# Performance work log

Measured on AMD Instinct MI355X. Metric: run time of the kernel, lower is better.

The kernel has to match this reference:

```python
import jax, jax.numpy as jnp
import numpy as np

BETA = 0.25
K = 1024   # num_codebook_vectors
D = 256    # latent_dim


def setup_inputs() -> dict:
    key = jax.random.key(0)
    k1, k2 = jax.random.split(key)
    z = jax.random.normal(k1, (32, D, 32, 32), dtype=jnp.float32)
    # original init: uniform(-1/K, 1/K)
    codebook = jax.random.uniform(k2, (K, D), dtype=jnp.float32, minval=-1.0 / K, maxval=1.0 / K)
    return {"z": z, "codebook": codebook}


def reference(z, codebook):
    B, C, H, W = z.shape
    sg = jax.lax.stop_gradient
    # NCHW -> NHWC, flatten to [N, D]
    z_nhwc = jnp.transpose(z, (0, 2, 3, 1))
    zf = z_nhwc.reshape(-1, C)
    # squared distances via sum-of-squares + matmul: [N, K]
    d = (jnp.sum(zf * zf, axis=1, keepdims=True)
         + jnp.sum(codebook * codebook, axis=1)
         - 2.0 * jnp.matmul(zf, codebook.T))
    idx = jnp.argmin(d, axis=1)                      # [N]
    z_q = codebook[idx].reshape(B, H, W, C)          # gather + reshape
    # commitment + codebook loss
    loss = (jnp.mean((sg(z_q) - z_nhwc) ** 2)
            + BETA * jnp.mean((z_q - sg(z_nhwc)) ** 2))
    # straight-through estimator
    z_q = z_nhwc + sg(z_q - z_nhwc)
    z_q = jnp.transpose(z_q, (0, 3, 1, 2))           # back to NCHW
    return z_q, idx, loss
```

## Files before the change

kernel.cpp:

```cpp
#include <hip/hip_runtime.h>

constexpr int D_ = 256;
constexpr int K_ = 1024;
constexpr int P_ = 1024;
constexpr int N_ = 32768;

constexpr int IDX_OFF  = 8388608;
constexpr int LOSS_OFF = 8421376;

constexpr int CB16_OFF = 0;
constexpr int CN_OFF   = 262400;
constexpr int ZN_OFF   = 263424;
constexpr int CNT_OFF  = 296448;
constexpr int WL_OFF   = 296449;

constexpr float RESCUE_MARGIN = 1e-4f;

typedef _Float16 half8 __attribute__((ext_vector_type(8)));
typedef float f32x4 __attribute__((ext_vector_type(4)));

__device__ __forceinline__ void stage16(const float* g, float* l) {
  __builtin_amdgcn_global_load_lds(
      (const __attribute__((address_space(1))) unsigned int*)g,
      (__attribute__((address_space(3))) unsigned int*)l, 16, 0, 0);
}

__global__ __launch_bounds__(64) void vq_prep(const float* __restrict__ z,
                                              const float* __restrict__ cb,
                                              float* __restrict__ scratch,
                                              float* __restrict__ loss) {
  const int blk = blockIdx.x;
  const int lane = threadIdx.x;
  if (blk < 512) {
    const int n0 = blk * 64;
    const int b = n0 >> 10, p0 = n0 & (P_ - 1);
    const float* zp = z + (size_t)b * (D_ * P_) + p0 + lane;
    float a8[8];
    #pragma unroll
    for (int i = 0; i < 8; ++i) a8[i] = 0.0f;
    for (int oct = 0; oct < 32; ++oct) {
      #pragma unroll
      for (int i = 0; i < 8; ++i) {
        float v = zp[(size_t)(oct * 8 + i) * P_];
        a8[i] = fmaf(v, v, a8[i]);
      }
    }
    scratch[ZN_OFF + n0 + lane] = ((a8[0] + a8[1]) + (a8[2] + a8[3])) +
                                  ((a8[4] + a8[5]) + (a8[6] + a8[7]));
    if (blk == 0 && lane == 0) {
      *loss = 0.0f;
      ((int*)(scratch + CNT_OFF))[0] = 0;
    }
  } else if (blk < 1536) {
    const int k = blk - 512;
    const float* row = cb + (size_t)k * D_;
    double s = 0.0;
    #pragma unroll
    for (int i = 0; i < 4; ++i) {
      double v = (double)row[lane + i * 64];
      s = fma(v, v, s);
    }
    #pragma unroll
    for (int off = 32; off; off >>= 1) s += __shfl_down(s, off, 64);
    if (lane == 0) scratch[CN_OFF + k] = (float)s;
  } else {
    const int kt = blk - 1536;
    const int k = kt * 16 + (lane & 15);
    const int quad = lane >> 4;
    _Float16* cw = (_Float16*)(scratch + CB16_OFF);
    for (int ds = 0; ds < 8; ++ds) {
      const float* src = cb + (size_t)k * D_ + ds * 32 + quad * 8;
      half8 h, lo;
      #pragma unroll
      for (int j = 0; j < 8; ++j) {
        const float v = src[j] * 1024.0f;
        const _Float16 hh = (_Float16)v;
        h[j] = hh;
        lo[j] = (_Float16)(v - (float)hh);
      }
      const int s = kt * 8 + ds;
      *(half8*)(cw + ((size_t)(s * 2 + 0) * 64 + lane) * 8) = h;
      *(half8*)(cw + ((size_t)(s * 2 + 1) * 64 + lane) * 8) = lo;
    }
  }
}

__global__ __launch_bounds__(256, 2) void vq_mfma(const float* __restrict__ z,
                                                  float* __restrict__ scratch,
                                                  float* __restrict__ idxf) {
  const int t = threadIdx.x;
  const int w = t >> 6;
  const int l = t & 63;
  const int quad = l >> 4;
  const int col = l & 15;
  const int n0 = blockIdx.x * 64;
  const int b = n0 >> 10;
  const int p0 = n0 & (P_ - 1);

  const float* __restrict__ cbsw_f = scratch + CB16_OFF;
  const float* __restrict__ cnorm = scratch + CN_OFF;
  const float* __restrict__ zn = scratch + ZN_OFF;

  __shared__ alignas(16) float Bbuf[3][4096];
  __shared__ alignas(16) float cnLds[1024];
  float* Azs = &Bbuf[2][0];

  *(float4*)(cnLds + t * 4) = *(const float4*)(cnorm + t * 4);

  const float4 znv = *(const float4*)(zn + n0 + w * 16 + quad * 4);
  float znr[4] = {znv.x, znv.y, znv.z, znv.w};

  half8 Ah[8], Al[8];
  const int pp = l;
  const int dl0 = w * 8;
  for (int ds = 0; ds < 8; ++ds) {
    __syncthreads();
    #pragma unroll
    for (int i = 0; i < 8; ++i) {
      const int dloc = dl0 + i;
      Azs[pp * 33 + dloc] =
          z[(size_t)b * (D_ * P_) + (size_t)(ds * 32 + dloc) * P_ + p0 + pp];
    }
    __syncthreads();
    {
      const int row_local = w * 16 + col;
      const float* src = &Azs[row_local * 33 + quad * 8];
      half8 h, lo;
      #pragma unroll
      for (int j = 0; j < 8; ++j) {
        const float v = src[j];
        const _Float16 hh = (_Float16)v;
        h[j] = hh;
        lo[j] = (_Float16)(v - (float)hh);
      }
      Ah[ds] = h;
      Al[ds] = lo;
    }
  }

  {
    const float* g0 = cbsw_f + l * 4;
    #pragma unroll
    for (int j = 0; j < 4; ++j) {
      const int chunk = w * 4 + j;
      stage16(g0 + chunk * 256, &Bbuf[0][chunk * 256]);
    }
    #pragma unroll
    for (int j = 0; j < 4; ++j) {
      const int chunk = w * 4 + j;
      stage16(g0 + 4096 + chunk * 256, &Bbuf[1][chunk * 256]);
    }
  }

  float m1[4], m2v[4];
  int i1[4];
  #pragma unroll
  for (int r = 0; r < 4; ++r) { m1[r] = 1e30f; m2v[r] = 1e30f; i1[r] = 0; }

  int cur = 0, stg = 2;
  const float* gs = cbsw_f + 2 * 4096 + l * 4;

  for (int kt = 0; kt < 64; ++kt) {
    if (kt < 63) {
      asm volatile("s_waitcnt vmcnt(4)" ::: "memory");
    } else {
      asm volatile("s_waitcnt vmcnt(0)" ::: "memory");
    }
    __builtin_amdgcn_s_barrier();
    __builtin_amdgcn_sched_barrier(0);

    if (kt < 62) {
      float* db = &Bbuf[stg][0];
      #pragma unroll
      for (int j = 0; j < 4; ++j) {
        const int chunk = w * 4 + j;
        stage16(gs + chunk * 256, db + chunk * 256);
      }
      gs += 4096;
    }

    const float* bb = &Bbuf[cur][0];
    const float cnf = cnLds[(kt << 4) + col];
    f32x4 a0 = {0.f, 0.f, 0.f, 0.f};
    f32x4 a1 = {0.f, 0.f, 0.f, 0.f};

    __builtin_amdgcn_s_setprio(1);
    #pragma unroll
    for (int ds = 0; ds < 4; ++ds) {
      const half8 bh = *(const half8*)(bb + (ds * 2 + 0) * 256 + l * 4);
      const half8 bl = *(const half8*)(bb + (ds * 2 + 1) * 256 + l * 4);
      a0 = __builtin_amdgcn_mfma_f32_16x16x32_f16(Ah[ds], bh, a0, 0, 0, 0);
      a0 = __builtin_amdgcn_mfma_f32_16x16x32_f16(Ah[ds], bl, a0, 0, 0, 0);
      a0 = __builtin_amdgcn_mfma_f32_16x16x32_f16(Al[ds], bh, a0, 0, 0, 0);
    }
    #pragma unroll
    for (int ds = 4; ds < 8; ++ds) {
      const half8 bh = *(const half8*)(bb + (ds * 2 + 0) * 256 + l * 4);
      const half8 bl = *(const half8*)(bb + (ds * 2 + 1) * 256 + l * 4);
      a1 = __builtin_amdgcn_mfma_f32_16x16x32_f16(Ah[ds], bh, a1, 0, 0, 0);
      a1 = __builtin_amdgcn_mfma_f32_16x16x32_f16(Ah[ds], bl, a1, 0, 0, 0);
      a1 = __builtin_amdgcn_mfma_f32_16x16x32_f16(Al[ds], bh, a1, 0, 0, 0);
    }
    __builtin_amdgcn_s_setprio(0);

    const int kg = (kt << 4) + col;
    #pragma unroll
    for (int r = 0; r < 4; ++r) {
      const float s0 = fmaf(a0[r] + a1[r], -0x1p-9f, znr[r] + cnf);
      if (s0 < m1[r]) { m2v[r] = m1[r]; m1[r] = s0; i1[r] = kg; }
      else if (s0 < m2v[r]) m2v[r] = s0;
    }

    cur = (cur == 2) ? 0 : cur + 1;
    stg = (stg == 2) ? 0 : stg + 1;
  }

  #pragma unroll
  for (int off = 1; off <= 8; off <<= 1) {
    #pragma unroll
    for (int r = 0; r < 4; ++r) {
      const float o1 = __shfl_xor(m1[r], off, 64);
      const float o2 = __shfl_xor(m2v[r], off, 64);
      const int oi = __shfl_xor(i1[r], off, 64);
      if (o1 < m1[r]) { m2v[r] = fminf(m1[r], o2); m1[r] = o1; i1[r] = oi; }
      else if (o1 == m1[r]) { i1[r] = min(i1[r], oi); m2v[r] = m1[r]; }
      else { m2v[r] = fminf(m2v[r], o1); }
    }
  }

  if (col == 0) {
    int* cnt = (int*)(scratch + CNT_OFF);
    int* wl = (int*)(scratch + WL_OFF);
    #pragma unroll
    for (int r = 0; r < 4; ++r) {
      const int n = n0 + w * 16 + quad * 4 + r;
      idxf[n] = (float)i1[r];
      if (m2v[r] - m1[r] < RESCUE_MARGIN) {
        const int pos = atomicAdd(cnt, 1);
        wl[pos] = n;
      }
    }
  }
}

__global__ __launch_bounds__(256, 4) void vq_rescue(const float* __restrict__ z,
                                                    const float* __restrict__ cb,
                                                    const float* __restrict__ scratch,
                                                    float* __restrict__ idxf) {
  const int tid = threadIdx.x;
  const float* cnorm = scratch + CN_OFF;
  const float* zn = scratch + ZN_OFF;
  const int count = ((const int*)(scratch + CNT_OFF))[0];
  const int* wl = (const int*)(scratch + WL_OFF);

  __shared__ alignas(16) float zb[8][D_];
  __shared__ int nrow[8];
  __shared__ float rv[256];
  __shared__ int ri[256];

  for (int base = blockIdx.x * 8; base < count; base += gridDim.x * 8) {
    const int take = min(8, count - base);
    if (tid < 8) nrow[tid] = wl[base + (tid < take ? tid : 0)];
    __syncthreads();
    #pragma unroll
    for (int r = 0; r < 8; ++r) {
      const int n = nrow[r];
      const int b = n >> 10, p = n & (P_ - 1);
      zb[r][tid] = z[(size_t)b * (D_ * P_) + (size_t)tid * P_ + p];
    }
    __syncthreads();

    const int k0 = tid * 4;
    const float4* __restrict__ cr0 = (const float4*)(cb + (size_t)(k0 + 0) * D_);
    const float4* __restrict__ cr1 = (const float4*)(cb + (size_t)(k0 + 1) * D_);
    const float4* __restrict__ cr2 = (const float4*)(cb + (size_t)(k0 + 2) * D_);
    const float4* __restrict__ cr3 = (const float4*)(cb + (size_t)(k0 + 3) * D_);

    float acc[8][4];
    #pragma unroll
    for (int r = 0; r < 8; ++r)
      #pragma unroll
      for (int j = 0; j < 4; ++j) acc[r][j] = 0.0f;

    for (int d4 = 0; d4 < 64; ++d4) {
      const float4 v0 = cr0[d4], v1 = cr1[d4], v2 = cr2[d4], v3 = cr3[d4];
      #pragma unroll
      for (int r = 0; r < 8; ++r) {
        const float4 zv = ((const float4*)zb[r])[d4];
        acc[r][0] = fmaf(zv.x, v0.x, acc[r][0]);
        acc[r][0] = fmaf(zv.y, v0.y, acc[r][0]);
        acc[r][0] = fmaf(zv.z, v0.z, acc[r][0]);
        acc[r][0] = fmaf(zv.w, v0.w, acc[r][0]);
        acc[r][1] = fmaf(zv.x, v1.x, acc[r][1]);
        acc[r][1] = fmaf(zv.y, v1.y, acc[r][1]);
        acc[r][1] = fmaf(zv.z, v1.z, acc[r][1]);
        acc[r][1] = fmaf(zv.w, v1.w, acc[r][1]);
        acc[r][2] = fmaf(zv.x, v2.x, acc[r][2]);
        acc[r][2] = fmaf(zv.y, v2.y, acc[r][2]);
        acc[r][2] = fmaf(zv.z, v2.z, acc[r][2]);
        acc[r][2] = fmaf(zv.w, v2.w, acc[r][2]);
        acc[r][3] = fmaf(zv.x, v3.x, acc[r][3]);
        acc[r][3] = fmaf(zv.y, v3.y, acc[r][3]);
        acc[r][3] = fmaf(zv.z, v3.z, acc[r][3]);
        acc[r][3] = fmaf(zv.w, v3.w, acc[r][3]);
      }
    }

    for (int r = 0; r < 8; ++r) {
      const int n = nrow[r];
      const float zA = zn[n];
      float bv = 1e30f;
      int bi = 0x7fffffff;
      #pragma unroll
      for (int j = 0; j < 4; ++j) {
        const float A = zA + cnorm[k0 + j];
        const float s = A - 2.0f * acc[r][j];
        if (s < bv) { bv = s; bi = k0 + j; }
      }
      rv[tid] = bv; ri[tid] = bi;
      __syncthreads();
      for (int off = 128; off >= 1; off >>= 1) {
        if (tid < off) {
          const float ov = rv[tid + off];
          const int oi = ri[tid + off];
          if (ov < rv[tid] || (ov == rv[tid] && oi < ri[tid])) { rv[tid] = ov; ri[tid] = oi; }
        }
        __syncthreads();
      }
      if (tid == 0 && r < take) idxf[n] = (float)ri[0];
      __syncthreads();
    }
  }
}

__global__ __launch_bounds__(256) void vq_gather(const float* __restrict__ z,
                                                 const float* __restrict__ cb,
                                                 const float* __restrict__ idxf,
                                                 float* __restrict__ out,
                                                 float* __restrict__ loss) {
  const int tid = threadIdx.x;
  const int lane = tid & 63;
  const int w = tid >> 6;
  const int n0 = blockIdx.x * 64;
  const int b = n0 >> 10;
  const int p0 = n0 & (P_ - 1);
  const int p = p0 + lane;

  const int idx = (int)(idxf[n0 + lane] + 0.5f);
  const float4* crow4 = (const float4*)(cb + (size_t)idx * D_);
  const size_t base = (size_t)b * (D_ * P_) + p;

  float acc = 0.0f;
  #pragma unroll 4
  for (int ci = 0; ci < 16; ++ci) {
    const float4 v = crow4[w * 16 + ci];
    const int c = w * 64 + ci * 4;
    const float vv[4] = {v.x, v.y, v.z, v.w};
    #pragma unroll
    for (int u = 0; u < 4; ++u) {
      const size_t a = base + (size_t)(c + u) * P_;
      const float zv = z[a];
      const float d = vv[u] - zv;
      out[a] = zv + d;
      acc = fmaf(d, d, acc);
    }
  }
  #pragma unroll
  for (int off = 32; off; off >>= 1) acc += __shfl_down(acc, off, 64);
  __shared__ float wsum[4];
  if (lane == 0) wsum[w] = acc;
  __syncthreads();
  if (tid == 0) {
    float s = wsum[0] + wsum[1] + wsum[2] + wsum[3];
    atomicAdd(loss, s * (1.25f / 8388608.0f));
  }
}

extern "C" void kernel_launch(void* const* d_in, const int* in_sizes, int n_in,
                              void* d_out, int out_size, void* d_ws, size_t ws_size,
                              hipStream_t stream) {
  const float* z = (const float*)d_in[0];
  const float* cb = (const float*)d_in[1];
  float* out = (float*)d_out;

  vq_prep<<<1600, 64, 0, stream>>>(z, cb, out, out + LOSS_OFF);
  vq_mfma<<<N_ / 64, 256, 0, stream>>>(z, out, out + IDX_OFF);
  vq_rescue<<<128, 256, 0, stream>>>(z, cb, out, out + IDX_OFF);
  vq_gather<<<N_ / 64, 256, 0, stream>>>(z, cb, out + IDX_OFF, out, out + LOSS_OFF);
}
```

Baseline: 251.5 us.

## Halve vq_mfma block to two waves each computing two row tiles

```diff
diff --git a/kernel.cpp b/kernel.cpp
--- a/kernel.cpp
+++ b/kernel.cpp
@@ -85,7 +85,7 @@
   }
 }
 
-__global__ __launch_bounds__(256, 2) void vq_mfma(const float* __restrict__ z,
+__global__ __launch_bounds__(128, 2) void vq_mfma(const float* __restrict__ z,
                                                   float* __restrict__ scratch,
                                                   float* __restrict__ idxf) {
   const int t = threadIdx.x;
@@ -105,26 +105,30 @@
   __shared__ alignas(16) float cnLds[1024];
   float* Azs = &Bbuf[2][0];
 
-  *(float4*)(cnLds + t * 4) = *(const float4*)(cnorm + t * 4);
-
-  const float4 znv = *(const float4*)(zn + n0 + w * 16 + quad * 4);
-  float znr[4] = {znv.x, znv.y, znv.z, znv.w};
-
-  half8 Ah[8], Al[8];
-  const int pp = l;
-  const int dl0 = w * 8;
+  *(float4*)(cnLds + t * 8)     = *(const float4*)(cnorm + t * 8);
+  *(float4*)(cnLds + t * 8 + 4) = *(const float4*)(cnorm + t * 8 + 4);
+
+  float znr[2][4];
+  #pragma unroll
+  for (int rt = 0; rt < 2; ++rt) {
+    const float4 znv = *(const float4*)(zn + n0 + w * 32 + rt * 16 + quad * 4);
+    znr[rt][0] = znv.x; znr[rt][1] = znv.y;
+    znr[rt][2] = znv.z; znr[rt][3] = znv.w;
+  }
+
+  half8 Ah[2][8], Al[2][8];
   for (int ds = 0; ds < 8; ++ds) {
     __syncthreads();
     #pragma unroll
-    for (int i = 0; i < 8; ++i) {
-      const int dloc = dl0 + i;
-      Azs[pp * 33 + dloc] =
-          z[(size_t)b * (D_ * P_) + (size_t)(ds * 32 + dloc) * P_ + p0 + pp];
+    for (int i = 0; i < 16; ++i) {
+      const int dloc = w * 16 + i;
+      Azs[l * 33 + dloc] =
+          z[(size_t)b * (D_ * P_) + (size_t)(ds * 32 + dloc) * P_ + p0 + l];
     }
     __syncthreads();
-    {
-      const int row_local = w * 16 + col;
-      const float* src = &Azs[row_local * 33 + quad * 8];
+    #pragma unroll
+    for (int rt = 0; rt < 2; ++rt) {
+      const float* src = &Azs[(w * 32 + rt * 16 + col) * 33 + quad * 8];
       half8 h, lo;
       #pragma unroll
       for (int j = 0; j < 8; ++j) {
@@ -133,36 +137,44 @@
         h[j] = hh;
         lo[j] = (_Float16)(v - (float)hh);
       }
-      Ah[ds] = h;
-      Al[ds] = lo;
-    }
-  }
+      Ah[rt][ds] = h;
+      Al[rt][ds] = lo;
+    }
+  }
+
+  asm volatile("s_waitcnt vmcnt(0)" ::: "memory");
 
   {
     const float* g0 = cbsw_f + l * 4;
     #pragma unroll
-    for (int j = 0; j < 4; ++j) {
-      const int chunk = w * 4 + j;
+    for (int j = 0; j < 8; ++j) {
+      const int chunk = w * 8 + j;
       stage16(g0 + chunk * 256, &Bbuf[0][chunk * 256]);
     }
     #pragma unroll
-    for (int j = 0; j < 4; ++j) {
-      const int chunk = w * 4 + j;
+    for (int j = 0; j < 8; ++j) {
+      const int chunk = w * 8 + j;
       stage16(g0 + 4096 + chunk * 256, &Bbuf[1][chunk * 256]);
     }
   }
 
-  float m1[4], m2v[4];
-  int i1[4];
+  float m1[2][4], m2v[2][4];
+  int i1[2][4];
   #pragma unroll
-  for (int r = 0; r < 4; ++r) { m1[r] = 1e30f; m2v[r] = 1e30f; i1[r] = 0; }
-
-  int cur = 0, stg = 2;
+  for (int rt = 0; rt < 2; ++rt)
+    #pragma unroll
+    for (int r = 0; r < 4; ++r) { m1[rt][r] = 1e30f; m2v[rt][r] = 1e30f; i1[rt][r] = 0; }
+
+  float* bp0 = &Bbuf[0][0];
+  float* bp1 = &Bbuf[1][0];
+  float* bp2 = &Bbuf[2][0];
   const float* gs = cbsw_f + 2 * 4096 + l * 4;
+  const float* cnp = cnLds;
+  int kg = col;
 
   for (int kt = 0; kt < 64; ++kt) {
     if (kt < 63) {
-      asm volatile("s_waitcnt vmcnt(4)" ::: "memory");
+      asm volatile("s_waitcnt vmcnt(8)" ::: "memory");
     } else {
       asm volatile("s_waitcnt vmcnt(0)" ::: "memory");
     }
@@ -170,76 +182,77 @@
     __builtin_amdgcn_sched_barrier(0);
 
     if (kt < 62) {
-      float* db = &Bbuf[stg][0];
-      #pragma unroll
-      for (int j = 0; j < 4; ++j) {
-        const int chunk = w * 4 + j;
-        stage16(gs + chunk * 256, db + chunk * 256);
+      #pragma unroll
+      for (int j = 0; j < 8; ++j) {
+        const int chunk = w * 8 + j;
+        stage16(gs + chunk * 256, bp2 + chunk * 256);
       }
       gs += 4096;
     }
 
-    const float* bb = &Bbuf[cur][0];
-    const float cnf = cnLds[(kt << 4) + col];
-    f32x4 a0 = {0.f, 0.f, 0.f, 0.f};
-    f32x4 a1 = {0.f, 0.f, 0.f, 0.f};
+    const float cnf = cnp[col];
+
+    f32x4 aH0 = {0.f,0.f,0.f,0.f}, aM0 = {0.f,0.f,0.f,0.f}, aL0 = {0.f,0.f,0.f,0.f};
+    f32x4 aH1 = {0.f,0.f,0.f,0.f}, aM1 = {0.f,0.f,0.f,0.f}, aL1 = {0.f,0.f,0.f,0.f};
 
     __builtin_amdgcn_s_setprio(1);
     #pragma unroll
-    for (int ds = 0; ds < 4; ++ds) {
-      const half8 bh = *(const half8*)(bb + (ds * 2 + 0) * 256 + l * 4);
-      const half8 bl = *(const half8*)(bb + (ds * 2 + 1) * 256 + l * 4);
-      a0 = __builtin_amdgcn_mfma_f32_16x16x32_f16(Ah[ds], bh, a0, 0, 0, 0);
-      a0 = __builtin_amdgcn_mfma_f32_16x16x32_f16(Ah[ds], bl, a0, 0, 0, 0);
-      a0 = __builtin_amdgcn_mfma_f32_16x16x32_f16(Al[ds], bh, a0, 0, 0, 0);
-    }
-    #pragma unroll
-    for (int ds = 4; ds < 8; ++ds) {
-      const half8 bh = *(const half8*)(bb + (ds * 2 + 0) * 256 + l * 4);
-      const half8 bl = *(const half8*)(bb + (ds * 2 + 1) * 256 + l * 4);
-      a1 = __builtin_amdgcn_mfma_f32_16x16x32_f16(Ah[ds], bh, a1, 0, 0, 0);
-      a1 = __builtin_amdgcn_mfma_f32_16x16x32_f16(Ah[ds], bl, a1, 0, 0, 0);
-      a1 = __builtin_amdgcn_mfma_f32_16x16x32_f16(Al[ds], bh, a1, 0, 0, 0);
+    for (int ds = 0; ds < 8; ++ds) {
+      const half8 bh = *(const half8*)(bp0 + (ds * 2 + 0) * 256 + l * 4);
+      const half8 bl = *(const half8*)(bp0 + (ds * 2 + 1) * 256 + l * 4);
+      aH0 = __builtin_amdgcn_mfma_f32_16x16x32_f16(Ah[0][ds], bh, aH0, 0, 0, 0);
+      aH1 = __builtin_amdgcn_mfma_f32_16x16x32_f16(Ah[1][ds], bh, aH1, 0, 0, 0);
+      aM0 = __builtin_amdgcn_mfma_f32_16x16x32_f16(Ah[0][ds], bl, aM0, 0, 0, 0);
+      aM1 = __builtin_amdgcn_mfma_f32_16x16x32_f16(Ah[1][ds], bl, aM1, 0, 0, 0);
+      aL0 = __builtin_amdgcn_mfma_f32_16x16x32_f16(Al[0][ds], bh, aL0, 0, 0, 0);
+      aL1 = __builtin_amdgcn_mfma_f32_16x16x32_f16(Al[1][ds], bh, aL1, 0, 0, 0);
     }
     __builtin_amdgcn_s_setprio(0);
 
-    const int kg = (kt << 4) + col;
     #pragma unroll
     for (int r = 0; r < 4; ++r) {
-      const float s0 = fmaf(a0[r] + a1[r], -0x1p-9f, znr[r] + cnf);
-      if (s0 < m1[r]) { m2v[r] = m1[r]; m1[r] = s0; i1[r] = kg; }
-      else if (s0 < m2v[r]) m2v[r] = s0;
-    }
-
-    cur = (cur == 2) ? 0 : cur + 1;
-    stg = (stg == 2) ? 0 : stg + 1;
+      const float s0 = fmaf((aH0[r] + aM0[r]) + aL0[r], -0x1p-9f, znr[0][r] + cnf);
+      if (s0 < m1[0][r]) { m2v[0][r] = m1[0][r]; m1[0][r] = s0; i1[0][r] = kg; }
+      else if (s0 < m2v[0][r]) m2v[0][r] = s0;
+      const float s1 = fmaf((aH1[r] + aM1[r]) + aL1[r], -0x1p-9f, znr[1][r] + cnf);
+      if (s1 < m1[1][r]) { m2v[1][r] = m1[1][r]; m1[1][r] = s1; i1[1][r] = kg; }
+      else if (s1 < m2v[1][r]) m2v[1][r] = s1;
+    }
+
+    cnp += 16;
+    kg += 16;
+    float* tmp = bp0; bp0 = bp1; bp1 = bp2; bp2 = tmp;
   }
 
   #pragma unroll
   for (int off = 1; off <= 8; off <<= 1) {
     #pragma unroll
-    for (int r = 0; r < 4; ++r) {
-      const float o1 = __shfl_xor(m1[r], off, 64);
-      const float o2 = __shfl_xor(m2v[r], off, 64);
-      const int oi = __shfl_xor(i1[r], off, 64);
-      if (o1 < m1[r]) { m2v[r] = fminf(m1[r], o2); m1[r] = o1; i1[r] = oi; }
-      else if (o1 == m1[r]) { i1[r] = min(i1[r], oi); m2v[r] = m1[r]; }
-      else { m2v[r] = fminf(m2v[r], o1); }
-    }
+    for (int rt = 0; rt < 2; ++rt)
+      #pragma unroll
+      for (int r = 0; r < 4; ++r) {
+        const float o1 = __shfl_xor(m1[rt][r], off, 64);
+        const float o2 = __shfl_xor(m2v[rt][r], off, 64);
+        const int oi = __shfl_xor(i1[rt][r], off, 64);
+        if (o1 < m1[rt][r]) { m2v[rt][r] = fminf(m1[rt][r], o2); m1[rt][r] = o1; i1[rt][r] = oi; }
+        else if (o1 == m1[rt][r]) { i1[rt][r] = min(i1[rt][r], oi); m2v[rt][r] = m1[rt][r]; }
+        else { m2v[rt][r] = fminf(m2v[rt][r], o1); }
+      }
   }
 
   if (col == 0) {
     int* cnt = (int*)(scratch + CNT_OFF);
     int* wl = (int*)(scratch + WL_OFF);
     #pragma unroll
-    for (int r = 0; r < 4; ++r) {
-      const int n = n0 + w * 16 + quad * 4 + r;
-      idxf[n] = (float)i1[r];
-      if (m2v[r] - m1[r] < RESCUE_MARGIN) {
-        const int pos = atomicAdd(cnt, 1);
-        wl[pos] = n;
-      }
-    }
+    for (int rt = 0; rt < 2; ++rt)
+      #pragma unroll
+      for (int r = 0; r < 4; ++r) {
+        const int n = n0 + w * 32 + rt * 16 + quad * 4 + r;
+        idxf[n] = (float)i1[rt][r];
+        if (m2v[rt][r] - m1[rt][r] < RESCUE_MARGIN) {
+          const int pos = atomicAdd(cnt, 1);
+          wl[pos] = n;
+        }
+      }
   }
 }
 
@@ -384,7 +397,7 @@
   float* out = (float*)d_out;
 
   vq_prep<<<1600, 64, 0, stream>>>(z, cb, out, out + LOSS_OFF);
-  vq_mfma<<<N_ / 64, 256, 0, stream>>>(z, out, out + IDX_OFF);
+  vq_mfma<<<N_ / 64, 128, 0, stream>>>(z, out, out + IDX_OFF);
   vq_rescue<<<128, 256, 0, stream>>>(z, cb, out, out + IDX_OFF);
   vq_gather<<<N_ / 64, 256, 0, stream>>>(z, cb, out + IDX_OFF, out, out + LOSS_OFF);
 }
```

Measured after the change: 267.5 us. +6.4%, slower.
